# Optimization experiments

Hardware: AMD Instinct MI355X
Metric: run time of the kernel (lower is better)

Reference implementation:

```python
import jax, jax.numpy as jnp
import numpy as np


def setup_inputs() -> dict:
    key = jax.random.key(0)
    k1, k2, k3, k4 = jax.random.split(key, 4)
    B, T, N, D = 4, 8, 512, 256
    BT = B * T
    x = jax.random.normal(k1, (BT, N, D), dtype=jnp.float32)
    A_causal = jax.random.uniform(k2, (B, N, N), dtype=jnp.float32)
    W_qkv = jax.random.normal(k3, (3 * D, D), dtype=jnp.float32) * (D ** -0.5)
    W_proj = jax.random.normal(k4, (D, D), dtype=jnp.float32) * (D ** -0.5)
    b_proj = jnp.zeros((D,), dtype=jnp.float32)
    causal_lambda = jnp.ones((1,), dtype=jnp.float32) * 0.1
    return {
        "x": x,
        "A_causal": A_causal,
        "W_qkv": W_qkv,
        "W_proj": W_proj,
        "b_proj": b_proj,
        "causal_lambda": causal_lambda,
        "num_frames": 8,
    }


def reference(x, A_causal, W_qkv, W_proj, b_proj, causal_lambda, num_frames):
    BT, N, D = x.shape
    H = 8
    hd = D // H
    scale = hd ** -0.5
    # qkv projection (torch Linear: x @ W.T), split into q,k,v of shape [BT,H,N,hd]
    qkv = (x @ W_qkv.T).reshape(BT, N, 3, H, hd)
    qkv = jnp.transpose(qkv, (2, 0, 3, 1, 4))  # [3,BT,H,N,hd]
    q, k, v = qkv[0], qkv[1], qkv[2]
    attn = jnp.einsum("bhnd,bhmd->bhnm", q, k) * scale  # [BT,H,N,N]
    # expand A_causal [B,N,N] over frames (axis 0) and heads (broadcast axis 1)
    A_exp = jnp.repeat(A_causal, num_frames, axis=0)[:, None, :, :]  # [BT,1,N,N]
    attn = attn + causal_lambda[0] * A_exp
    attn = jax.nn.softmax(attn, axis=-1)
    out = jnp.einsum("bhnm,bhmd->bhnd", attn, v)  # [BT,H,N,hd]
    out = jnp.transpose(out, (0, 2, 1, 3)).reshape(BT, N, D)
    return out @ W_proj.T + b_proj
```

## Files before the change

kernel.cpp:

```cpp
#include <hip/hip_runtime.h>
#include <hip/hip_bf16.h>

typedef unsigned short u16;
typedef unsigned int   u32;
typedef __attribute__((ext_vector_type(8))) short short8;
typedef __attribute__((ext_vector_type(4))) float f32x4;

static __device__ __forceinline__ u16 f2b(float f) {
    __hip_bfloat16 h = __float2bfloat16(f);
    return *reinterpret_cast<u16*>(&h);
}
static __device__ __forceinline__ u32 pk2(float a, float b) {
    return (u32)f2b(a) | ((u32)f2b(b) << 16);
}

#define LDK 72

__global__ __launch_bounds__(256) void prep(const float* __restrict__ X,
                                            const float* __restrict__ A,
                                            const float* __restrict__ LAM,
                                            const float* __restrict__ Wq,
                                            const float* __restrict__ Wp,
                                            u16* __restrict__ xb,
                                            u16* __restrict__ AB,
                                            u16* __restrict__ wqb,
                                            u16* __restrict__ wpb) {
    const int bid = blockIdx.x;
    const float* src;
    u16* dst;
    float scale;
    int base;
    if (bid < 2048)      { src = X;  dst = xb;  scale = 1.0f;   base = bid * 2048; }
    else if (bid < 2560) { src = A;  dst = AB;  scale = LAM[0]; base = (bid - 2048) * 2048; }
    else if (bid < 2656) { src = Wq; dst = wqb; scale = 1.0f;   base = (bid - 2560) * 2048; }
    else                 { src = Wp; dst = wpb; scale = 1.0f;   base = (bid - 2656) * 2048; }
    const int i = base + threadIdx.x * 8;
    const float4 a = *(const float4*)(src + i);
    const float4 b = *(const float4*)(src + i + 4);
    uint4 o;
    o.x = pk2(scale * a.x, scale * a.y);
    o.y = pk2(scale * a.z, scale * a.w);
    o.z = pk2(scale * b.x, scale * b.y);
    o.w = pk2(scale * b.z, scale * b.w);
    *(uint4*)(dst + i) = o;
}

__global__ __launch_bounds__(256) void qkv_gemm(const u16* __restrict__ XB,
                                                const u16* __restrict__ WB,
                                                u16* __restrict__ qo,
                                                u16* __restrict__ ko,
                                                u16* __restrict__ vt) {
    __shared__ u16 SH[2 * 128 * LDK];
    u16* Xs = SH;
    u16* Ws = SH + 128 * LDK;
    const int t    = threadIdx.x;
    const int m0   = blockIdx.x << 7;
    const int o0   = blockIdx.y << 7;
    const int lane = t & 63;
    const int wid  = t >> 6;
    const int wr   = (wid >> 1) << 6;
    const int wc   = (wid & 1) << 6;
    const int ln   = lane & 15;
    const int quad = lane >> 4;

    const int r  = t >> 1;
    const int hf = (t & 1) << 5;
    const u16* xg = XB + (size_t)(m0 + r) * 256 + hf;
    const u16* wg = WB + (size_t)(o0 + r) * 256 + hf;
    uint4* xls = (uint4*)&Xs[r * LDK + hf];
    uint4* wls = (uint4*)&Ws[r * LDK + hf];

    f32x4 acc[4][4] = {};

    for (int kc = 0; kc < 256; kc += 64) {
        const uint4* xp = (const uint4*)(xg + kc);
        const uint4* wp = (const uint4*)(wg + kc);
        uint4 x0 = xp[0], x1 = xp[1], x2 = xp[2], x3 = xp[3];
        uint4 w0 = wp[0], w1 = wp[1], w2 = wp[2], w3 = wp[3];
        __syncthreads();
        xls[0] = x0; xls[1] = x1; xls[2] = x2; xls[3] = x3;
        wls[0] = w0; wls[1] = w1; wls[2] = w2; wls[3] = w3;
        __syncthreads();
#pragma unroll
        for (int kk = 0; kk < 64; kk += 32) {
            short8 a[4], b[4];
#pragma unroll
            for (int i = 0; i < 4; ++i)
                a[i] = *(const short8*)&Xs[(wr + i * 16 + ln) * LDK + kk + quad * 8];
#pragma unroll
            for (int j = 0; j < 4; ++j)
                b[j] = *(const short8*)&Ws[(wc + j * 16 + ln) * LDK + kk + quad * 8];
#pragma unroll
            for (int i = 0; i < 4; ++i)
#pragma unroll
                for (int j = 0; j < 4; ++j)
                    acc[i][j] = __builtin_amdgcn_mfma_f32_16x16x32_bf16(a[i], b[j], acc[i][j], 0, 0, 0);
        }
    }

    const int which = o0 >> 8;
    if (which < 2) {
        const float qscale = (which == 0) ? 0.17677669529663689f : 1.0f;
        u16* dst = (which == 0) ? qo : ko;
#pragma unroll
        for (int i = 0; i < 4; ++i) {
            const int mb = m0 + wr + i * 16 + quad * 4;
#pragma unroll
            for (int j = 0; j < 4; ++j) {
                const int o   = o0 + wc + j * 16 + ln;
                const int rem = o & 255;
                const int hh  = rem >> 5;
                const int dd  = rem & 31;
#pragma unroll
                for (int rr = 0; rr < 4; ++rr) {
                    const int m  = mb + rr;
                    const int bt = m >> 9;
                    const int n  = m & 511;
                    dst[(((size_t)bt * 8 + hh) * 512 + n) * 32 + dd] = f2b(acc[i][j][rr] * qscale);
                }
            }
        }
    } else {
        __syncthreads();
        u16* T = SH;
#pragma unroll
        for (int i = 0; i < 4; ++i) {
            const int ml = wr + i * 16 + quad * 4;
#pragma unroll
            for (int j = 0; j < 4; ++j) {
                const int ol = wc + j * 16 + ln;
                uint2 pv;
                pv.x = pk2(acc[i][j][0], acc[i][j][1]);
                pv.y = pk2(acc[i][j][2], acc[i][j][3]);
                *(uint2*)&T[ol * 136 + ml] = pv;
            }
        }
        __syncthreads();
        const int row = t >> 1;
        const int seg = (t & 1) << 6;
        const int o   = o0 + row;
        const int rem = o & 255;
        const int hh  = rem >> 5;
        const int dd  = rem & 31;
        const int bt  = m0 >> 9;
        u16* dstv = vt + (((size_t)bt * 8 + hh) * 32 + dd) * 512 + (m0 & 511) + seg;
#pragma unroll
        for (int kk2 = 0; kk2 < 8; ++kk2) {
            uint4 val = *(const uint4*)&T[row * 136 + seg + kk2 * 8];
            *(uint4*)(dstv + kk2 * 8) = val;
        }
    }
}

__global__ __launch_bounds__(256, 4) void attn_mfma(const u16* __restrict__ Q,
                                                    const u16* __restrict__ K,
                                                    const u16* __restrict__ VT,
                                                    const u16* __restrict__ AB,
                                                    const int* __restrict__ NF,
                                                    u16* __restrict__ AO) {
    __shared__ u16 Ks[2][64 * 40];
    __shared__ u16 Vs[2][32 * 72];
    __shared__ u16 Ps[4][32 * 40];
    const int t    = threadIdx.x;
    const int w    = t >> 6;
    const int lane = t & 63;
    const int ln   = lane & 15;
    const int quad = lane >> 4;
    const int L    = blockIdx.x;
    const int rr_  = L >> 3;
    const int qt   = rr_ & 3;
    const int h    = (rr_ >> 2) & 7;
    const int bt   = (L & 7) * 4 + (rr_ >> 5);
    const int bh   = bt * 8 + h;
    const int q0   = qt * 128 + w * 32;
    const size_t base = (size_t)bh * (512 * 32);
    const int b    = bt / NF[0];
    const u16* Ab  = AB + (size_t)b * 512 * 512;
    const u16* Ar0 = Ab + (size_t)(q0 + ln) * 512 + quad * 4;
    const u16* Ar1 = Ab + (size_t)(q0 + 16 + ln) * 512 + quad * 4;

    const int krow = t >> 2, kcol = (t & 3) * 8;
    const int vd   = t >> 3, vn   = (t & 7) * 8;
    const u16* Kg = K + base;
    const u16* Vg = VT + base;

    {
        uint4 s0 = *(const uint4*)(Kg + (size_t)krow * 32 + kcol);
        uint4 s2 = *(const uint4*)(Vg + (size_t)vd * 512 + vn);
        *(uint4*)&Ks[0][krow * 40 + kcol] = s0;
        *(uint4*)&Vs[0][vd * 72 + vn]     = s2;
    }
    uint2 ar[8];
#pragma unroll
    for (int mt = 0; mt < 4; ++mt) {
        ar[2*mt]     = *(const uint2*)(Ar0 + mt * 16);
        ar[2*mt + 1] = *(const uint2*)(Ar1 + mt * 16);
    }

    short8 qf[2];
#pragma unroll
    for (int nt = 0; nt < 2; ++nt)
        qf[nt] = *(const short8*)(Q + base + (size_t)(q0 + nt * 16 + ln) * 32 + quad * 8);

    f32x4 o[2][2] = {};
    float lsum0 = 0.f, lsum1 = 0.f;
    __syncthreads();

    int cur = 0;
    for (int jt = 0; jt < 512; jt += 64) {
        const int nxt = cur ^ 1;
        const int jn  = (jt + 64) & 511;
        uint4 t0 = *(const uint4*)(Kg + (size_t)(jn + krow) * 32 + kcol);
        uint4 t2 = *(const uint4*)(Vg + (size_t)vd * 512 + jn + vn);
        uint2 arn[8];
#pragma unroll
        for (int mt = 0; mt < 4; ++mt) {
            arn[2*mt]     = *(const uint2*)(Ar0 + jn + mt * 16);
            arn[2*mt + 1] = *(const uint2*)(Ar1 + jn + mt * 16);
        }

        float ps0 = 0.f, ps1 = 0.f;
#pragma unroll
        for (int ks = 0; ks < 2; ++ks) {
#pragma unroll
            for (int mm = 0; mm < 2; ++mm) {
                const int mt = 2 * ks + mm;
                short8 ka = *(const short8*)&Ks[cur][(mt * 16 + ln) * 40 + quad * 8];
                f32x4 c0, c1;
                c0[0] = __uint_as_float(ar[2*mt].x << 16);   c0[1] = __uint_as_float(ar[2*mt].x & 0xffff0000u);
                c0[2] = __uint_as_float(ar[2*mt].y << 16);   c0[3] = __uint_as_float(ar[2*mt].y & 0xffff0000u);
                c1[0] = __uint_as_float(ar[2*mt+1].x << 16); c1[1] = __uint_as_float(ar[2*mt+1].x & 0xffff0000u);
                c1[2] = __uint_as_float(ar[2*mt+1].y << 16); c1[3] = __uint_as_float(ar[2*mt+1].y & 0xffff0000u);
                const f32x4 s0 = __builtin_amdgcn_mfma_f32_16x16x32_bf16(ka, qf[0], c0, 0, 0, 0);
                const f32x4 s1 = __builtin_amdgcn_mfma_f32_16x16x32_bf16(ka, qf[1], c1, 0, 0, 0);
                const float p00 = __expf(s0[0]), p01 = __expf(s0[1]), p02 = __expf(s0[2]), p03 = __expf(s0[3]);
                const float p10 = __expf(s1[0]), p11 = __expf(s1[1]), p12 = __expf(s1[2]), p13 = __expf(s1[3]);
                ps0 += (p00 + p01) + (p02 + p03);
                ps1 += (p10 + p11) + (p12 + p13);
                uint2 w0; w0.x = pk2(p00, p01); w0.y = pk2(p02, p03);
                uint2 w1; w1.x = pk2(p10, p11); w1.y = pk2(p12, p13);
                *(uint2*)&Ps[w][ln * 40 + mm * 16 + quad * 4]        = w0;
                *(uint2*)&Ps[w][(16 + ln) * 40 + mm * 16 + quad * 4] = w1;
            }
            short8 pa0 = *(const short8*)&Ps[w][ln * 40 + quad * 8];
            short8 pa1 = *(const short8*)&Ps[w][(16 + ln) * 40 + quad * 8];
            short8 vb0 = *(const short8*)&Vs[cur][ln * 72 + ks * 32 + quad * 8];
            short8 vb1 = *(const short8*)&Vs[cur][(16 + ln) * 72 + ks * 32 + quad * 8];
            o[0][0] = __builtin_amdgcn_mfma_f32_16x16x32_bf16(pa0, vb0, o[0][0], 0, 0, 0);
            o[0][1] = __builtin_amdgcn_mfma_f32_16x16x32_bf16(pa0, vb1, o[0][1], 0, 0, 0);
            o[1][0] = __builtin_amdgcn_mfma_f32_16x16x32_bf16(pa1, vb0, o[1][0], 0, 0, 0);
            o[1][1] = __builtin_amdgcn_mfma_f32_16x16x32_bf16(pa1, vb1, o[1][1], 0, 0, 0);
        }

        *(uint4*)&Ks[nxt][krow * 40 + kcol] = t0;
        *(uint4*)&Vs[nxt][vd * 72 + vn]     = t2;
        ps0 += __shfl_xor(ps0, 16); ps0 += __shfl_xor(ps0, 32); lsum0 += ps0;
        ps1 += __shfl_xor(ps1, 16); ps1 += __shfl_xor(ps1, 32); lsum1 += ps1;
        __syncthreads();
#pragma unroll
        for (int i = 0; i < 8; ++i) ar[i] = arn[i];
        cur = nxt;
    }

#pragma unroll
    for (int r = 0; r < 4; ++r) {
        const int src = quad * 4 + r;
        const float i0 = 1.f / __shfl(lsum0, src);
        const float i1 = 1.f / __shfl(lsum1, src);
        const int n0 = qt * 128 + w * 32 + quad * 4 + r;
#pragma unroll
        for (int ntd = 0; ntd < 2; ++ntd) {
            AO[((size_t)bt * 512 + n0) * 256 + h * 32 + ntd * 16 + ln]      = f2b(o[0][ntd][r] * i0);
            AO[((size_t)bt * 512 + n0 + 16) * 256 + h * 32 + ntd * 16 + ln] = f2b(o[1][ntd][r] * i1);
        }
    }
}

__global__ __launch_bounds__(256) void proj_gemm(const u16* __restrict__ X,
                                                 const u16* __restrict__ WB,
                                                 const float* __restrict__ BIAS,
                                                 float* __restrict__ OUT) {
    __shared__ u16 Xs[128 * LDK];
    __shared__ u16 Ws[128 * LDK];
    const int t    = threadIdx.x;
    const int m0   = blockIdx.x << 7;
    const int o0   = blockIdx.y << 7;
    const int lane = t & 63;
    const int wid  = t >> 6;
    const int wr   = (wid >> 1) << 6;
    const int wc   = (wid & 1) << 6;
    const int ln   = lane & 15;
    const int quad = lane >> 4;

    const int r  = t >> 1;
    const int hf = (t & 1) << 5;
    const u16* xg = X + (size_t)(m0 + r) * 256 + hf;
    const u16* wg = WB + (size_t)(o0 + r) * 256 + hf;
    uint4* xls = (uint4*)&Xs[r * LDK + hf];
    uint4* wls = (uint4*)&Ws[r * LDK + hf];

    f32x4 acc[4][4] = {};

    for (int kc = 0; kc < 256; kc += 64) {
        const uint4* xp = (const uint4*)(xg + kc);
        const uint4* wp = (const uint4*)(wg + kc);
        uint4 x0 = xp[0], x1 = xp[1], x2 = xp[2], x3 = xp[3];
        uint4 w0 = wp[0], w1 = wp[1], w2 = wp[2], w3 = wp[3];
        __syncthreads();
        xls[0] = x0; xls[1] = x1; xls[2] = x2; xls[3] = x3;
        wls[0] = w0; wls[1] = w1; wls[2] = w2; wls[3] = w3;
        __syncthreads();
#pragma unroll
        for (int kk = 0; kk < 64; kk += 32) {
            short8 a[4], b[4];
#pragma unroll
            for (int i = 0; i < 4; ++i)
                a[i] = *(const short8*)&Xs[(wr + i * 16 + ln) * LDK + kk + quad * 8];
#pragma unroll
            for (int j = 0; j < 4; ++j)
                b[j] = *(const short8*)&Ws[(wc + j * 16 + ln) * LDK + kk + quad * 8];
#pragma unroll
            for (int i = 0; i < 4; ++i)
#pragma unroll
                for (int j = 0; j < 4; ++j)
                    acc[i][j] = __builtin_amdgcn_mfma_f32_16x16x32_bf16(a[i], b[j], acc[i][j], 0, 0, 0);
        }
    }

#pragma unroll
    for (int i = 0; i < 4; ++i) {
        const int mb = m0 + wr + i * 16 + quad * 4;
#pragma unroll
        for (int j = 0; j < 4; ++j) {
            const int o  = o0 + wc + j * 16 + ln;
            const float bo = BIAS[o];
#pragma unroll
            for (int rr = 0; rr < 4; ++rr) {
                const int m = mb + rr;
                OUT[(size_t)m * 256 + o] = acc[i][j][rr] + bo;
            }
        }
    }
}

extern "C" void kernel_launch(void* const* d_in, const int* in_sizes, int n_in,
                              void* d_out, int out_size, void* d_ws, size_t ws_size,
                              hipStream_t stream) {
    (void)in_sizes; (void)n_in; (void)out_size; (void)ws_size;
    const float* x     = (const float*)d_in[0];
    const float* A     = (const float*)d_in[1];
    const float* Wqkv  = (const float*)d_in[2];
    const float* Wproj = (const float*)d_in[3];
    const float* bproj = (const float*)d_in[4];
    const float* lam   = (const float*)d_in[5];
    const int*   nf    = (const int*)d_in[6];
    float* out = (float*)d_out;

    u16* q   = (u16*)d_ws;
    u16* k   = q + 4194304;
    u16* vt  = k + 4194304;
    u16* ao  = vt + 4194304;
    u16* xb  = ao + 4194304;
    u16* AB  = xb + 4194304;
    u16* wqb = AB + 1048576;
    u16* wpb = wqb + 196608;

    prep     <<<dim3(2688), 256, 0, stream>>>(x, A, lam, Wqkv, Wproj, xb, AB, wqb, wpb);
    qkv_gemm <<<dim3(128, 6), 256, 0, stream>>>(xb, wqb, q, k, vt);
    attn_mfma<<<dim3(1024), 256, 0, stream>>>(q, k, vt, AB, nf, ao);
    proj_gemm<<<dim3(128, 2), 256, 0, stream>>>(ao, wpb, bproj, out);
}
```

Measured before the change: 144.4 us.

## Fuse fp32-to-bf16 conversion into GEMM loads and use exp2 softmax

After: 165.6 us. 1.15x slower.

```diff
diff --git a/kernel.cpp b/kernel.cpp
--- a/kernel.cpp
+++ b/kernel.cpp
@@ -6,50 +6,43 @@
 typedef __attribute__((ext_vector_type(8))) short short8;
 typedef __attribute__((ext_vector_type(4))) float f32x4;
 
+#define LOG2E 1.4426950408889634f
+#define LDK 72
+
 static __device__ __forceinline__ u16 f2b(float f) {
-    __hip_bfloat16 h = __float2bfloat16(f);
-    return *reinterpret_cast<u16*>(&h);
+    u32 u = __float_as_uint(f);
+    u += 0x7fffu + ((u >> 16) & 1u);
+    return (u16)(u >> 16);
 }
 static __device__ __forceinline__ u32 pk2(float a, float b) {
     return (u32)f2b(a) | ((u32)f2b(b) << 16);
 }
 
-#define LDK 72
-
-__global__ __launch_bounds__(256) void prep(const float* __restrict__ X,
-                                            const float* __restrict__ A,
-                                            const float* __restrict__ LAM,
-                                            const float* __restrict__ Wq,
-                                            const float* __restrict__ Wp,
-                                            u16* __restrict__ xb,
-                                            u16* __restrict__ AB,
-                                            u16* __restrict__ wqb,
-                                            u16* __restrict__ wpb) {
-    const int bid = blockIdx.x;
-    const float* src;
-    u16* dst;
-    float scale;
-    int base;
-    if (bid < 2048)      { src = X;  dst = xb;  scale = 1.0f;   base = bid * 2048; }
-    else if (bid < 2560) { src = A;  dst = AB;  scale = LAM[0]; base = (bid - 2048) * 2048; }
-    else if (bid < 2656) { src = Wq; dst = wqb; scale = 1.0f;   base = (bid - 2560) * 2048; }
-    else                 { src = Wp; dst = wpb; scale = 1.0f;   base = (bid - 2656) * 2048; }
-    const int i = base + threadIdx.x * 8;
-    const float4 a = *(const float4*)(src + i);
-    const float4 b = *(const float4*)(src + i + 4);
-    uint4 o;
-    o.x = pk2(scale * a.x, scale * a.y);
-    o.y = pk2(scale * a.z, scale * a.w);
-    o.z = pk2(scale * b.x, scale * b.y);
-    o.w = pk2(scale * b.z, scale * b.w);
-    *(uint4*)(dst + i) = o;
-}
-
-__global__ __launch_bounds__(256) void qkv_gemm(const u16* __restrict__ XB,
-                                                const u16* __restrict__ WB,
+__global__ __launch_bounds__(256) void qkv_gemm(const float* __restrict__ X,
+                                                const float* __restrict__ W,
+                                                const float* __restrict__ A,
+                                                const float* __restrict__ LAM,
                                                 u16* __restrict__ qo,
                                                 u16* __restrict__ ko,
-                                                u16* __restrict__ vt) {
+                                                u16* __restrict__ vt,
+                                                u16* __restrict__ AB) {
+    if (blockIdx.y == 6) {
+        const float s = LAM[0] * LOG2E;
+#pragma unroll
+        for (int c = 0; c < 4; ++c) {
+            const int i = blockIdx.x * 8192 + c * 2048 + threadIdx.x * 8;
+            const float4 a = *(const float4*)(A + i);
+            const float4 b = *(const float4*)(A + i + 4);
+            uint4 o;
+            o.x = pk2(s * a.x, s * a.y);
+            o.y = pk2(s * a.z, s * a.w);
+            o.z = pk2(s * b.x, s * b.y);
+            o.w = pk2(s * b.z, s * b.w);
+            *(uint4*)(AB + i) = o;
+        }
+        return;
+    }
+
     __shared__ u16 SH[2 * 128 * LDK];
     u16* Xs = SH;
     u16* Ws = SH + 128 * LDK;
@@ -65,21 +58,32 @@
 
     const int r  = t >> 1;
     const int hf = (t & 1) << 5;
-    const u16* xg = XB + (size_t)(m0 + r) * 256 + hf;
-    const u16* wg = WB + (size_t)(o0 + r) * 256 + hf;
+    const float* xg = X + (size_t)(m0 + r) * 256 + hf;
+    const float* wg = W + (size_t)(o0 + r) * 256 + hf;
     uint4* xls = (uint4*)&Xs[r * LDK + hf];
     uint4* wls = (uint4*)&Ws[r * LDK + hf];
 
     f32x4 acc[4][4] = {};
 
     for (int kc = 0; kc < 256; kc += 64) {
-        const uint4* xp = (const uint4*)(xg + kc);
-        const uint4* wp = (const uint4*)(wg + kc);
-        uint4 x0 = xp[0], x1 = xp[1], x2 = xp[2], x3 = xp[3];
-        uint4 w0 = wp[0], w1 = wp[1], w2 = wp[2], w3 = wp[3];
-        __syncthreads();
-        xls[0] = x0; xls[1] = x1; xls[2] = x2; xls[3] = x3;
-        wls[0] = w0; wls[1] = w1; wls[2] = w2; wls[3] = w3;
+        const float4* xp = (const float4*)(xg + kc);
+        const float4* wp = (const float4*)(wg + kc);
+        uint4 xo[4], wo[4];
+#pragma unroll
+        for (int j = 0; j < 4; ++j) {
+            const float4 a = xp[2 * j], b = xp[2 * j + 1];
+            xo[j].x = pk2(a.x, a.y); xo[j].y = pk2(a.z, a.w);
+            xo[j].z = pk2(b.x, b.y); xo[j].w = pk2(b.z, b.w);
+        }
+#pragma unroll
+        for (int j = 0; j < 4; ++j) {
+            const float4 a = wp[2 * j], b = wp[2 * j + 1];
+            wo[j].x = pk2(a.x, a.y); wo[j].y = pk2(a.z, a.w);
+            wo[j].z = pk2(b.x, b.y); wo[j].w = pk2(b.z, b.w);
+        }
+        __syncthreads();
+#pragma unroll
+        for (int j = 0; j < 4; ++j) { xls[j] = xo[j]; wls[j] = wo[j]; }
         __syncthreads();
 #pragma unroll
         for (int kk = 0; kk < 64; kk += 32) {
@@ -100,7 +104,7 @@
 
     const int which = o0 >> 8;
     if (which < 2) {
-        const float qscale = (which == 0) ? 0.17677669529663689f : 1.0f;
+        const float qscale = (which == 0) ? 0.17677669529663689f * LOG2E : 1.0f;
         u16* dst = (which == 0) ? qo : ko;
 #pragma unroll
         for (int i = 0; i < 4; ++i) {
@@ -233,8 +237,10 @@
                 c1[2] = __uint_as_float(ar[2*mt+1].y << 16); c1[3] = __uint_as_float(ar[2*mt+1].y & 0xffff0000u);
                 const f32x4 s0 = __builtin_amdgcn_mfma_f32_16x16x32_bf16(ka, qf[0], c0, 0, 0, 0);
                 const f32x4 s1 = __builtin_amdgcn_mfma_f32_16x16x32_bf16(ka, qf[1], c1, 0, 0, 0);
-                const float p00 = __expf(s0[0]), p01 = __expf(s0[1]), p02 = __expf(s0[2]), p03 = __expf(s0[3]);
-                const float p10 = __expf(s1[0]), p11 = __expf(s1[1]), p12 = __expf(s1[2]), p13 = __expf(s1[3]);
+                const float p00 = __builtin_amdgcn_exp2f(s0[0]), p01 = __builtin_amdgcn_exp2f(s0[1]);
+                const float p02 = __builtin_amdgcn_exp2f(s0[2]), p03 = __builtin_amdgcn_exp2f(s0[3]);
+                const float p10 = __builtin_amdgcn_exp2f(s1[0]), p11 = __builtin_amdgcn_exp2f(s1[1]);
+                const float p12 = __builtin_amdgcn_exp2f(s1[2]), p13 = __builtin_amdgcn_exp2f(s1[3]);
                 ps0 += (p00 + p01) + (p02 + p03);
                 ps1 += (p10 + p11) + (p12 + p13);
                 uint2 w0; w0.x = pk2(p00, p01); w0.y = pk2(p02, p03);
@@ -277,7 +283,7 @@
 }
 
 __global__ __launch_bounds__(256) void proj_gemm(const u16* __restrict__ X,
-                                                 const u16* __restrict__ WB,
+                                                 const float* __restrict__ W,
                                                  const float* __restrict__ BIAS,
                                                  float* __restrict__ OUT) {
     __shared__ u16 Xs[128 * LDK];
@@ -294,21 +300,28 @@
 
     const int r  = t >> 1;
     const int hf = (t & 1) << 5;
-    const u16* xg = X + (size_t)(m0 + r) * 256 + hf;
-    const u16* wg = WB + (size_t)(o0 + r) * 256 + hf;
+    const u16*   xg = X + (size_t)(m0 + r) * 256 + hf;
+    const float* wg = W + (size_t)(o0 + r) * 256 + hf;
     uint4* xls = (uint4*)&Xs[r * LDK + hf];
     uint4* wls = (uint4*)&Ws[r * LDK + hf];
 
     f32x4 acc[4][4] = {};
 
     for (int kc = 0; kc < 256; kc += 64) {
-        const uint4* xp = (const uint4*)(xg + kc);
-        const uint4* wp = (const uint4*)(wg + kc);
+        const uint4*  xp = (const uint4*)(xg + kc);
+        const float4* wp = (const float4*)(wg + kc);
         uint4 x0 = xp[0], x1 = xp[1], x2 = xp[2], x3 = xp[3];
-        uint4 w0 = wp[0], w1 = wp[1], w2 = wp[2], w3 = wp[3];
+        uint4 wo[4];
+#pragma unroll
+        for (int j = 0; j < 4; ++j) {
+            const float4 a = wp[2 * j], b = wp[2 * j + 1];
+            wo[j].x = pk2(a.x, a.y); wo[j].y = pk2(a.z, a.w);
+            wo[j].z = pk2(b.x, b.y); wo[j].w = pk2(b.z, b.w);
+        }
         __syncthreads();
         xls[0] = x0; xls[1] = x1; xls[2] = x2; xls[3] = x3;
-        wls[0] = w0; wls[1] = w1; wls[2] = w2; wls[3] = w3;
+#pragma unroll
+        for (int j = 0; j < 4; ++j) wls[j] = wo[j];
         __syncthreads();
 #pragma unroll
         for (int kk = 0; kk < 64; kk += 32) {
@@ -354,19 +367,16 @@
     const float* bproj = (const float*)d_in[4];
     const float* lam   = (const float*)d_in[5];
     const int*   nf    = (const int*)d_in[6];
+
     float* out = (float*)d_out;
 
     u16* q   = (u16*)d_ws;
     u16* k   = q + 4194304;
     u16* vt  = k + 4194304;
     u16* ao  = vt + 4194304;
-    u16* xb  = ao + 4194304;
-    u16* AB  = xb + 4194304;
-    u16* wqb = AB + 1048576;
-    u16* wpb = wqb + 196608;
-
-    prep     <<<dim3(2688), 256, 0, stream>>>(x, A, lam, Wqkv, Wproj, xb, AB, wqb, wpb);
-    qkv_gemm <<<dim3(128, 6), 256, 0, stream>>>(xb, wqb, q, k, vt);
+    u16* AB  = ao + 4194304;
+
+    qkv_gemm <<<dim3(128, 7), 256, 0, stream>>>(x, Wqkv, A, lam, q, k, vt, AB);
     attn_mfma<<<dim3(1024), 256, 0, stream>>>(q, k, vt, AB, nf, ao);
-    proj_gemm<<<dim3(128, 2), 256, 0, stream>>>(ao, wpb, bproj, out);
-}
+    proj_gemm<<<dim3(128, 2), 256, 0, stream>>>(ao, Wproj, bproj, out);
+}
```
